# Kernel optimization log

Measured on AMD Instinct MI355X. Metric: run time of the kernel, lower is better.

The kernel has to match this reference:

```python
import jax, jax.numpy as jnp
import numpy as np

N = 100000
E = 1000000
NODE_DIM = 128
EDGE_DIM = 32
HID = 64
HIER = 32
NUM_CLASS = 10
NUM_LAYERS = 3
BN_EPS = 1e-5


def setup_inputs() -> dict:
    key = jax.random.key(0)
    ks = jax.random.split(key, 16)
    s = 0.05
    return {
        "x": jax.random.normal(ks[0], (N, NODE_DIM), jnp.float32),
        "e": jax.random.normal(ks[1], (E, EDGE_DIM), jnp.float32),
        "c": jax.random.normal(ks[2], (N, HIER), jnp.float32),
        "w_node": jax.random.normal(ks[3], (NODE_DIM, HID), jnp.float32) * s,
        "b_node": jnp.zeros((HID,), jnp.float32),
        "w_edge": jax.random.normal(ks[4], (EDGE_DIM, HID), jnp.float32) * s,
        "b_edge": jnp.zeros((HID,), jnp.float32),
        "w_out1": jax.random.normal(ks[5], (HIER + HID, 2 * HID), jnp.float32) * s,
        "b_out1": jnp.zeros((2 * HID,), jnp.float32),
        "bn_gamma": jnp.ones((2 * HID,), jnp.float32),
        "bn_beta": jnp.zeros((2 * HID,), jnp.float32),
        "prelu_a": jnp.asarray(0.25, jnp.float32),
        "w_out2": jax.random.normal(ks[6], (2 * HID, NUM_CLASS), jnp.float32) * s,
        "b_out2": jnp.zeros((NUM_CLASS,), jnp.float32),
        "edge_index": jax.random.randint(ks[7], (2, E), 0, N, jnp.int64),
    }


def reference(x, e, c, w_node, b_node, w_edge, b_edge, w_out1, b_out1,
              bn_gamma, bn_beta, prelu_a, w_out2, b_out2, edge_index):
    n = x.shape[0]
    h = x @ w_node + b_node                      # [N, HID]
    eh = e @ w_edge + b_edge                     # [E, HID]
    src, dst = edge_index[0], edge_index[1]
    loop = jnp.arange(n)
    # add_self_loops + zero self-loop edge_attr (done inside each GCN layer,
    # identical every layer so hoisted)
    src_f = jnp.concatenate([src, loop])
    dst_f = jnp.concatenate([dst, loop])
    e_f = jnp.concatenate([eh, jnp.zeros((n, eh.shape[1]), eh.dtype)], axis=0)
    deg = jax.ops.segment_sum(jnp.ones(dst_f.shape, x.dtype), dst_f, num_segments=n)
    dinv = deg ** -0.5                           # deg >= 1 thanks to self loops
    norm = (dinv[src_f] * dinv[dst_f])[:, None]  # [E+N, 1]
    h_sum = h
    for _ in range(NUM_LAYERS):
        msg = norm * (h[src_f] + e_f)            # gather + edge compute
        h = jax.ops.segment_sum(msg, dst_f, num_segments=n)  # scatter-add
        h = jax.nn.leaky_relu(h, 0.2)
        h_sum = h_sum + h                        # sum over h_list
    z = jnp.concatenate([h_sum, c], axis=-1) @ w_out1 + b_out1
    # BatchNorm1d (training-mode batch statistics, biased variance)
    mu = z.mean(axis=0)
    var = z.var(axis=0)
    z = (z - mu) / jnp.sqrt(var + BN_EPS) * bn_gamma + bn_beta
    z = jnp.where(z > 0, z, prelu_a * z)         # PReLU (single param)
    return z @ w_out2 + b_out2
```

## Files before the change

kernel.cpp:

```cpp
#include <hip/hip_runtime.h>
#include <math.h>

#define N_NODES 100000
#define N_EDGES 1000000
#define HID     64
#define HIER    32
#define NDIM    128
#define EDIM    32
#define K1      96
#define C1      128
#define NCLS    10
#define BN_EPS  1e-5f
#define SCAN_B  98
#define ZTILES  782
#define HTILES2 782

__device__ __forceinline__ unsigned pk_bf16(float a, float b) {
    unsigned ua = __float_as_uint(a);
    ua = (ua + 0x7FFFu + ((ua >> 16) & 1u)) >> 16;
    unsigned ub = __float_as_uint(b);
    ub = (ub + 0x7FFFu + ((ub >> 16) & 1u)) & 0xFFFF0000u;
    return ua | ub;
}
__device__ __forceinline__ float bf_lo(unsigned g) { return __uint_as_float(g << 16); }
__device__ __forceinline__ float bf_hi(unsigned g) { return __uint_as_float(g & 0xFFFF0000u); }


__global__ void k_count(const int* __restrict__ ei, int* __restrict__ cnt) {
    int i = blockIdx.x * blockDim.x + threadIdx.x;
    if (i < N_EDGES) atomicAdd(&cnt[ei[N_EDGES + i]], 1);
}

__global__ void k_scan1(const int* __restrict__ cnt, int* __restrict__ offs,
                        float* __restrict__ dinv, int* __restrict__ bsum) {
    __shared__ int buf[2][1024];
    int t = threadIdx.x, b = blockIdx.x;
    int i = b * 1024 + t;
    int v = (i < N_NODES) ? cnt[i] : 0;
    buf[0][t] = v; __syncthreads();
    int pi = 0;
    for (int off = 1; off < 1024; off <<= 1) {
        int x = buf[pi][t];
        if (t >= off) x += buf[pi][t - off];
        buf[pi ^ 1][t] = x; __syncthreads(); pi ^= 1;
    }
    int incl = buf[pi][t];
    if (i < N_NODES) {
        offs[i] = incl - v;
        dinv[i] = rsqrtf((float)(v + 1));
    }
    if (t == 1023) bsum[b] = incl;
}

__global__ void k_scan2(int* __restrict__ bsum, int nb) {
    __shared__ int buf[2][1024];
    int t = threadIdx.x;
    int v = (t < nb) ? bsum[t] : 0;
    buf[0][t] = v; __syncthreads();
    int pi = 0;
    for (int off = 1; off < 1024; off <<= 1) {
        int x = buf[pi][t];
        if (t >= off) x += buf[pi][t - off];
        buf[pi ^ 1][t] = x; __syncthreads(); pi ^= 1;
    }
    int incl = buf[pi][t];
    if (t < nb) bsum[t] = incl - v;
}

__global__ void k_scan3(const int* __restrict__ bsum, int* __restrict__ offs) {
    int b = blockIdx.x;
    int i = b * 1024 + threadIdx.x;
    if (i < N_NODES) offs[i] += bsum[b];
    if (i == 0) offs[N_NODES] = N_EDGES;
}

__global__ void k_fill(const int* __restrict__ ei, const int* __restrict__ offs,
                       int* __restrict__ cursor, const float* __restrict__ dinv,
                       int4* __restrict__ epk) {
    int i = blockIdx.x * blockDim.x + threadIdx.x;
    if (i >= N_EDGES) return;
    int s = ei[i], d = ei[N_EDGES + i];
    int pos = offs[d] + atomicAdd(&cursor[d], 1);
    epk[pos] = make_int4(s, i, __float_as_int(dinv[s]), 0);
}


__global__ __launch_bounds__(256) void k_conv(const float4* __restrict__ e4,
                                              uint4* __restrict__ eb4) {
    int i = blockIdx.x * 256 + threadIdx.x;
    float4 a = e4[(size_t)2 * i];
    float4 b = e4[(size_t)2 * i + 1];
    uint4 pk;
    pk.x = pk_bf16(a.x, a.y); pk.y = pk_bf16(a.z, a.w);
    pk.z = pk_bf16(b.x, b.y); pk.w = pk_bf16(b.z, b.w);
    eb4[i] = pk;
}

__global__ __launch_bounds__(256) void k_conv2(const float4* __restrict__ c4,
                                               uint2* __restrict__ cb2) {
    int i = blockIdx.x * 256 + threadIdx.x;
    if (i >= N_NODES * 8) return;
    float4 a = c4[i];
    cb2[i] = make_uint2(pk_bf16(a.x, a.y), pk_bf16(a.z, a.w));
}


__global__ __launch_bounds__(256) void k_agg3(const unsigned* __restrict__ ebfu,
                                              const int4* __restrict__ epk,
                                              const int* __restrict__ offs,
                                              const float* __restrict__ dinv,
                                              float* __restrict__ agg,
                                              float* __restrict__ wsumv) {
    int v = (blockIdx.x * 256 + threadIdx.x) >> 4;
    if (v >= N_NODES) return;
    int q = threadIdx.x & 15;
    int start = offs[v], end = offs[v + 1];
    float ax = 0.f, ay = 0.f, wacc = 0.f;
    for (int i = start; i < end; i += 4) {
        int i1 = i + 1, i2 = i + 2, i3 = i + 3;
        int4 p0 = epk[i];
        int4 p1 = (i1 < end) ? epk[i1] : make_int4(0, 0, 0, 0);
        int4 p2 = (i2 < end) ? epk[i2] : make_int4(0, 0, 0, 0);
        int4 p3 = (i3 < end) ? epk[i3] : make_int4(0, 0, 0, 0);
        float n0 = __int_as_float(p0.z), n1 = __int_as_float(p1.z);
        float n2 = __int_as_float(p2.z), n3 = __int_as_float(p3.z);
        unsigned g0 = ebfu[(size_t)p0.y * 16 + q];
        unsigned g1 = ebfu[(size_t)p1.y * 16 + q];
        unsigned g2 = ebfu[(size_t)p2.y * 16 + q];
        unsigned g3 = ebfu[(size_t)p3.y * 16 + q];
        ax += n0 * bf_lo(g0) + n1 * bf_lo(g1) + n2 * bf_lo(g2) + n3 * bf_lo(g3);
        ay += n0 * bf_hi(g0) + n1 * bf_hi(g1) + n2 * bf_hi(g2) + n3 * bf_hi(g3);
        wacc += n0 + n1 + n2 + n3;
    }
    float dv = dinv[v];
    *(float2*)&agg[(size_t)v * EDIM + q * 2] = make_float2(dv * ax, dv * ay);
    if (q == 0) wsumv[v] = dv * wacc;
}


__global__ __launch_bounds__(256) void k_h0t2(const float* __restrict__ x,
                                              const float* __restrict__ w,
                                              const float* __restrict__ bias,
                                              unsigned* __restrict__ hbf) {
    __shared__ __align__(16) unsigned wpk[NDIM * 36];
    __shared__ float xt[128 * 33];
    for (int i = threadIdx.x; i < NDIM * 32; i += 256) {
        int k = i >> 5, j = i & 31;
        wpk[k * 36 + j] = pk_bf16(w[k * HID + 2 * j], w[k * HID + 2 * j + 1]);
    }
    int tid = threadIdx.x;
    int lane = tid & 63, wave = tid >> 6;
    int lr = lane >> 3, lc = lane & 7;
    int rbase = wave * 32 + lr * 4;
    int cbase = lc * 8;
    float bA[8];
    #pragma unroll
    for (int j = 0; j < 8; ++j) bA[j] = bias[cbase + j];
    for (int tile = blockIdx.x; tile < HTILES2; tile += gridDim.x) {
        int row0 = tile * 128;
        float acc[4][8];
        #pragma unroll
        for (int i = 0; i < 4; ++i)
            #pragma unroll
            for (int j = 0; j < 8; ++j) acc[i][j] = 0.f;
        for (int ch = 0; ch < 4; ++ch) {
            __syncthreads();
            #pragma unroll
            for (int p = 0; p < 4; ++p) {
                int idx = p * 256 + tid;
                int row = idx >> 3, kq = idx & 7;
                int gk = ch * 32 + kq * 4;
                float4 v = make_float4(0.f, 0.f, 0.f, 0.f);
                int gr = row0 + row;
                if (gr < N_NODES) v = *(const float4*)&x[(size_t)gr * NDIM + gk];
                float* d = &xt[row * 33 + kq * 4];
                d[0] = v.x; d[1] = v.y; d[2] = v.z; d[3] = v.w;
            }
            __syncthreads();
            for (int k = 0; k < 32; ++k) {
                float u[4];
                #pragma unroll
                for (int i = 0; i < 4; ++i) u[i] = xt[(rbase + i) * 33 + k];
                uint4 wp = *(const uint4*)&wpk[(ch * 32 + k) * 36 + lc * 4];
                float wv[8];
                wv[0] = bf_lo(wp.x); wv[1] = bf_hi(wp.x);
                wv[2] = bf_lo(wp.y); wv[3] = bf_hi(wp.y);
                wv[4] = bf_lo(wp.z); wv[5] = bf_hi(wp.z);
                wv[6] = bf_lo(wp.w); wv[7] = bf_hi(wp.w);
                #pragma unroll
                for (int i = 0; i < 4; ++i)
                    #pragma unroll
                    for (int j = 0; j < 8; ++j) acc[i][j] += u[i] * wv[j];
            }
        }
        #pragma unroll
        for (int i = 0; i < 4; ++i) {
            int gr = row0 + rbase + i;
            if (gr < N_NODES) {
                uint4 pk;
                pk.x = pk_bf16(acc[i][0] + bA[0], acc[i][1] + bA[1]);
                pk.y = pk_bf16(acc[i][2] + bA[2], acc[i][3] + bA[3]);
                pk.z = pk_bf16(acc[i][4] + bA[4], acc[i][5] + bA[5]);
                pk.w = pk_bf16(acc[i][6] + bA[6], acc[i][7] + bA[7]);
                *(uint4*)&hbf[(size_t)gr * 32 + (cbase >> 1)] = pk;
            }
        }
    }
}


__global__ __launch_bounds__(256) void k_se(const float* __restrict__ agg,
                                            const float* __restrict__ wsumv,
                                            const float* __restrict__ we,
                                            const float* __restrict__ be,
                                            unsigned* __restrict__ sebf) {
    int lane = threadIdx.x & 63, wid = threadIdx.x >> 6;
    float wreg[EDIM];
    #pragma unroll
    for (int k = 0; k < EDIM; ++k) wreg[k] = we[k * HID + lane];
    float bl = be[lane];
    for (int v = blockIdx.x * 4 + wid; v < N_NODES; v += gridDim.x * 4) {
        const float4* ar = (const float4*)(agg + (size_t)v * EDIM);
        float acc = wsumv[v] * bl;
        #pragma unroll
        for (int k4 = 0; k4 < EDIM / 4; ++k4) {
            float4 av = ar[k4];
            int k = k4 * 4;
            acc += av.x * wreg[k + 0] + av.y * wreg[k + 1] +
                   av.z * wreg[k + 2] + av.w * wreg[k + 3];
        }
        float partner = __shfl_xor(acc, 1);
        if ((lane & 1) == 0)
            sebf[(size_t)v * 32 + (lane >> 1)] = pk_bf16(acc, partner);
    }
}


__global__ __launch_bounds__(256) void k_layer4(const unsigned* __restrict__ hold,
                                                const unsigned* __restrict__ sebf,
                                                const int4* __restrict__ epk,
                                                const int* __restrict__ offs,
                                                const float* __restrict__ dinv,
                                                unsigned* __restrict__ hnew) {
    int v = (blockIdx.x * 256 + threadIdx.x) >> 4;
    if (v >= N_NODES) return;
    int q = threadIdx.x & 15;
    int start = offs[v], end = offs[v + 1];
    float dv = dinv[v];
    size_t vp = (size_t)v * 16 + q;
    uint2 hv = ((const uint2*)hold)[vp];
    float a0 = dv * bf_lo(hv.x), a1 = dv * bf_hi(hv.x);
    float a2 = dv * bf_lo(hv.y), a3 = dv * bf_hi(hv.y);
    for (int i = start; i < end; i += 8) {
        int idx[8]; float nn[8]; uint2 gg[8];
        #pragma unroll
        for (int u = 0; u < 8; ++u) {
            int ii = i + u;
            int4 p = (ii < end) ? epk[ii] : make_int4(0, 0, 0, 0);
            idx[u] = p.x;
            nn[u]  = __int_as_float(p.z);
        }
        #pragma unroll
        for (int u = 0; u < 8; ++u) gg[u] = ((const uint2*)hold)[(size_t)idx[u] * 16 + q];
        #pragma unroll
        for (int u = 0; u < 8; ++u) {
            a0 += nn[u] * bf_lo(gg[u].x); a1 += nn[u] * bf_hi(gg[u].x);
            a2 += nn[u] * bf_lo(gg[u].y); a3 += nn[u] * bf_hi(gg[u].y);
        }
    }
    uint2 sv = ((const uint2*)sebf)[vp];
    float r0 = bf_lo(sv.x) + dv * a0;
    float r1 = bf_hi(sv.x) + dv * a1;
    float r2 = bf_lo(sv.y) + dv * a2;
    float r3 = bf_hi(sv.y) + dv * a3;
    r0 = (r0 > 0.f) ? r0 : 0.2f * r0;
    r1 = (r1 > 0.f) ? r1 : 0.2f * r1;
    r2 = (r2 > 0.f) ? r2 : 0.2f * r2;
    r3 = (r3 > 0.f) ? r3 : 0.2f * r3;
    ((uint2*)hnew)[vp] = make_uint2(pk_bf16(r0, r1), pk_bf16(r2, r3));
}

__global__ __launch_bounds__(256) void k_layer4s(const unsigned* __restrict__ hold,
                                                 const unsigned* __restrict__ hb0,
                                                 const unsigned* __restrict__ hb1,
                                                 const unsigned* __restrict__ sebf,
                                                 const int4* __restrict__ epk,
                                                 const int* __restrict__ offs,
                                                 const float* __restrict__ dinv,
                                                 unsigned* __restrict__ hnew,
                                                 unsigned* __restrict__ hsbf) {
    int v = (blockIdx.x * 256 + threadIdx.x) >> 4;
    if (v >= N_NODES) return;
    int q = threadIdx.x & 15;
    int start = offs[v], end = offs[v + 1];
    float dv = dinv[v];
    size_t vp = (size_t)v * 16 + q;
    uint2 hv = ((const uint2*)hold)[vp];
    float a0 = dv * bf_lo(hv.x), a1 = dv * bf_hi(hv.x);
    float a2 = dv * bf_lo(hv.y), a3 = dv * bf_hi(hv.y);
    for (int i = start; i < end; i += 8) {
        int idx[8]; float nn[8]; uint2 gg[8];
        #pragma unroll
        for (int u = 0; u < 8; ++u) {
            int ii = i + u;
            int4 p = (ii < end) ? epk[ii] : make_int4(0, 0, 0, 0);
            idx[u] = p.x;
            nn[u]  = __int_as_float(p.z);
        }
        #pragma unroll
        for (int u = 0; u < 8; ++u) gg[u] = ((const uint2*)hold)[(size_t)idx[u] * 16 + q];
        #pragma unroll
        for (int u = 0; u < 8; ++u) {
            a0 += nn[u] * bf_lo(gg[u].x); a1 += nn[u] * bf_hi(gg[u].x);
            a2 += nn[u] * bf_lo(gg[u].y); a3 += nn[u] * bf_hi(gg[u].y);
        }
    }
    uint2 sv = ((const uint2*)sebf)[vp];
    float r0 = bf_lo(sv.x) + dv * a0;
    float r1 = bf_hi(sv.x) + dv * a1;
    float r2 = bf_lo(sv.y) + dv * a2;
    float r3 = bf_hi(sv.y) + dv * a3;
    r0 = (r0 > 0.f) ? r0 : 0.2f * r0;
    r1 = (r1 > 0.f) ? r1 : 0.2f * r1;
    r2 = (r2 > 0.f) ? r2 : 0.2f * r2;
    r3 = (r3 > 0.f) ? r3 : 0.2f * r3;
    ((uint2*)hnew)[vp] = make_uint2(pk_bf16(r0, r1), pk_bf16(r2, r3));
    uint2 g0 = ((const uint2*)hb0)[vp];
    uint2 g1 = ((const uint2*)hb1)[vp];
    float s0 = r0 + bf_lo(g0.x) + bf_lo(g1.x) + bf_lo(hv.x);
    float s1 = r1 + bf_hi(g0.x) + bf_hi(g1.x) + bf_hi(hv.x);
    float s2 = r2 + bf_lo(g0.y) + bf_lo(g1.y) + bf_lo(hv.y);
    float s3 = r3 + bf_hi(g0.y) + bf_hi(g1.y) + bf_hi(hv.y);
    ((uint2*)hsbf)[vp] = make_uint2(pk_bf16(s0, s1), pk_bf16(s2, s3));
}


__global__ __launch_bounds__(256) void k_zstats(const unsigned* __restrict__ hsbf,
                                                const unsigned* __restrict__ cbf,
                                                const float* __restrict__ w1,
                                                const float* __restrict__ b1,
                                                unsigned* __restrict__ zbf,
                                                float* __restrict__ stats) {
    __shared__ __align__(16) unsigned wpk[K1 * 68];
    __shared__ __align__(16) unsigned ut[K1 * 68];
    __shared__ float red[4][64];
    for (int i = threadIdx.x; i < K1 * 64; i += 256) {
        int k = i >> 6, j = i & 63;
        wpk[k * 68 + j] = pk_bf16(w1[k * C1 + 2 * j], w1[k * C1 + 2 * j + 1]);
    }
    int tid = threadIdx.x;
    int lane = tid & 63, wave = tid >> 6;
    int lr = lane >> 3, lc = lane & 7;
    int wr = wave >> 1, wc = wave & 1;
    int rbase = wr * 64 + lr * 8;
    int cbase = wc * 64 + lc * 8;
    int kslot = wave;
    int rp = lane;
    float bA[8];
    #pragma unroll
    for (int j = 0; j < 8; ++j) bA[j] = b1[cbase + j];
    float s[8], q[8];
    #pragma unroll
    for (int j = 0; j < 8; ++j) { s[j] = 0.f; q[j] = 0.f; }

    for (int tile = blockIdx.x; tile < ZTILES; tile += gridDim.x) {
        int row0 = tile * 128;
        __syncthreads();
        {
            int r0g = row0 + 2 * rp, r1g = r0g + 1;
            bool ok0 = r0g < N_NODES, ok1 = r1g < N_NODES;
            #pragma unroll
            for (int kku = 0; kku < 12; ++kku) {
                int ku = kslot * 12 + kku;
                unsigned A = 0u, B = 0u;
                if (ku < 32) {
                    if (ok0) A = hsbf[(size_t)r0g * 32 + ku];
                    if (ok1) B = hsbf[(size_t)r1g * 32 + ku];
                } else {
                    if (ok0) A = cbf[(size_t)r0g * 16 + (ku - 32)];
                    if (ok1) B = cbf[(size_t)r1g * 16 + (ku - 32)];
                }
                int k0 = 2 * ku;
                ut[k0 * 68 + rp]       = (A & 0xFFFFu) | (B << 16);
                ut[(k0 + 1) * 68 + rp] = (A >> 16) | (B & 0xFFFF0000u);
            }
        }
        __syncthreads();
        float acc[8][8];
        #pragma unroll
        for (int i = 0; i < 8; ++i)
            #pragma unroll
            for (int j = 0; j < 8; ++j) acc[i][j] = 0.f;
        for (int k = 0; k < K1; ++k) {
            uint4 up = *(const uint4*)&ut[k * 68 + wr * 32 + lr * 4];
            uint4 wp = *(const uint4*)&wpk[k * 68 + wc * 32 + lc * 4];
            float u[8], wv[8];
            u[0] = bf_lo(up.x); u[1] = bf_hi(up.x);
            u[2] = bf_lo(up.y); u[3] = bf_hi(up.y);
            u[4] = bf_lo(up.z); u[5] = bf_hi(up.z);
            u[6] = bf_lo(up.w); u[7] = bf_hi(up.w);
            wv[0] = bf_lo(wp.x); wv[1] = bf_hi(wp.x);
            wv[2] = bf_lo(wp.y); wv[3] = bf_hi(wp.y);
            wv[4] = bf_lo(wp.z); wv[5] = bf_hi(wp.z);
            wv[6] = bf_lo(wp.w); wv[7] = bf_hi(wp.w);
            #pragma unroll
            for (int i = 0; i < 8; ++i) {
                acc[i][0] += u[i] * wv[0]; acc[i][1] += u[i] * wv[1];
                acc[i][2] += u[i] * wv[2]; acc[i][3] += u[i] * wv[3];
                acc[i][4] += u[i] * wv[4]; acc[i][5] += u[i] * wv[5];
                acc[i][6] += u[i] * wv[6]; acc[i][7] += u[i] * wv[7];
            }
        }
        #pragma unroll
        for (int i = 0; i < 8; ++i) {
            int gr = row0 + rbase + i;
            if (gr < N_NODES) {
                float zz[8];
                #pragma unroll
                for (int j = 0; j < 8; ++j) {
                    zz[j] = acc[i][j] + bA[j];
                    s[j] += zz[j]; q[j] += zz[j] * zz[j];
                }
                uint4 pk;
                pk.x = pk_bf16(zz[0], zz[1]); pk.y = pk_bf16(zz[2], zz[3]);
                pk.z = pk_bf16(zz[4], zz[5]); pk.w = pk_bf16(zz[6], zz[7]);
                *(uint4*)&zbf[(size_t)gr * 64 + (cbase >> 1)] = pk;
            }
        }
    }

    #pragma unroll
    for (int j = 0; j < 8; ++j) {
        s[j] += __shfl_xor(s[j], 8); s[j] += __shfl_xor(s[j], 16); s[j] += __shfl_xor(s[j], 32);
        q[j] += __shfl_xor(q[j], 8); q[j] += __shfl_xor(q[j], 16); q[j] += __shfl_xor(q[j], 32);
    }
    __syncthreads();
    if (lr == 0) {
        #pragma unroll
        for (int j = 0; j < 8; ++j) red[wave][lc * 8 + j] = s[j];
    }
    __syncthreads();
    if (tid < 128) {
        int wc2 = tid >> 6, cl = tid & 63;
        atomicAdd(&stats[wc2 * 64 + cl], red[wc2][cl] + red[wc2 + 2][cl]);
    }
    __syncthreads();
    if (lr == 0) {
        #pragma unroll
        for (int j = 0; j < 8; ++j) red[wave][lc * 8 + j] = q[j];
    }
    __syncthreads();
    if (tid < 128) {
        int wc2 = tid >> 6, cl = tid & 63;
        atomicAdd(&stats[C1 + wc2 * 64 + cl], red[wc2][cl] + red[wc2 + 2][cl]);
    }
}

__global__ void k_ab(const float* __restrict__ stats, const float* __restrict__ gamma,
                     const float* __restrict__ beta, float* __restrict__ ab) {
    int t = threadIdx.x;
    if (t < C1) {
        float mu = stats[t] / (float)N_NODES;
        float var = stats[C1 + t] / (float)N_NODES - mu * mu;
        float inv = rsqrtf(var + BN_EPS);
        float a = gamma[t] * inv;
        ab[t] = a;
        ab[C1 + t] = beta[t] - mu * a;
    }
}


__global__ __launch_bounds__(256) void k_out3(const unsigned* __restrict__ zbf,
                                              const float* __restrict__ ab,
                                              const float* __restrict__ pa,
                                              const float* __restrict__ w2,
                                              const float* __restrict__ b2,
                                              float* __restrict__ out) {
    int v = blockIdx.x * 256 + threadIdx.x;
    if (v >= N_NODES) return;
    float alpha = pa[0];
    float acc[NCLS];
    #pragma unroll
    for (int j = 0; j < NCLS; ++j) acc[j] = b2[j];
    const uint4* zr = (const uint4*)(zbf + (size_t)v * 64);
    #pragma unroll
    for (int pk4 = 0; pk4 < 16; ++pk4) {
        uint4 g = zr[pk4];
        unsigned gw[4] = {g.x, g.y, g.z, g.w};
        #pragma unroll
        for (int w = 0; w < 4; ++w) {
            int d0 = pk4 * 8 + w * 2;
            float p0 = bf_lo(gw[w]) * ab[d0]     + ab[C1 + d0];
            float p1 = bf_hi(gw[w]) * ab[d0 + 1] + ab[C1 + d0 + 1];
            p0 = (p0 > 0.f) ? p0 : alpha * p0;
            p1 = (p1 > 0.f) ? p1 : alpha * p1;
            #pragma unroll
            for (int j = 0; j < NCLS; ++j)
                acc[j] += p0 * w2[d0 * NCLS + j] + p1 * w2[(d0 + 1) * NCLS + j];
        }
    }
    #pragma unroll
    for (int j = 0; j < NCLS; ++j) out[(size_t)v * NCLS + j] = acc[j];
}


extern "C" void kernel_launch(void* const* d_in, const int* in_sizes, int n_in,
                              void* d_out, int out_size, void* d_ws, size_t ws_size,
                              hipStream_t stream) {
    const float* x      = (const float*)d_in[0];
    const float* e      = (const float*)d_in[1];
    const float* c      = (const float*)d_in[2];
    const float* w_node = (const float*)d_in[3];
    const float* b_node = (const float*)d_in[4];
    const float* w_edge = (const float*)d_in[5];
    const float* b_edge = (const float*)d_in[6];
    const float* w_out1 = (const float*)d_in[7];
    const float* b_out1 = (const float*)d_in[8];
    const float* gamma  = (const float*)d_in[9];
    const float* beta   = (const float*)d_in[10];
    const float* pa     = (const float*)d_in[11];
    const float* w_out2 = (const float*)d_in[12];
    const float* b_out2 = (const float*)d_in[13];
    const int*   ei     = (const int*)d_in[14];
    float* out = (float*)d_out;

    char* wsb = (char*)d_ws;
    ushort*   ebf  = (ushort*)wsb;
    unsigned* sebf = (unsigned*)wsb;
    unsigned* zbf  = (unsigned*)(wsb + 12800000);
    size_t off = (64000000 + 255) & ~(size_t)255;
    auto alloc = [&](size_t bytes) {
        void* p = wsb + off;
        off = (off + bytes + 255) & ~(size_t)255;
        return p;
    };
    int*      cnt      = (int*)alloc(4ull * N_NODES);
    int*      offs     = (int*)alloc(4ull * (N_NODES + 1));
    float*    dinv     = (float*)alloc(4ull * N_NODES);
    int*      bsum     = (int*)alloc(4ull * 128);
    int4*     epk      = (int4*)alloc(16ull * N_EDGES);
    float*    agg      = (float*)alloc(4ull * N_NODES * EDIM);
    float*    wsumv    = (float*)alloc(4ull * N_NODES);
    float*    stats    = (float*)alloc(4ull * 256);
    float*    ab       = (float*)alloc(4ull * 256);
    unsigned* hb0      = (unsigned*)alloc(4ull * N_NODES * 32);
    unsigned* hb1      = (unsigned*)alloc(4ull * N_NODES * 32);
    unsigned* hb2      = (unsigned*)alloc(4ull * N_NODES * 32);
    unsigned* hb3      = (unsigned*)alloc(4ull * N_NODES * 32);
    unsigned* cbf      = (unsigned*)alloc(4ull * N_NODES * 16);
    unsigned* hsbf     = (unsigned*)agg;

    hipMemsetAsync(cnt, 0, 4ull * N_NODES, stream);
    hipMemsetAsync(stats, 0, 4ull * 256, stream);

    k_count<<<(N_EDGES + 255) / 256, 256, 0, stream>>>(ei, cnt);
    k_scan1<<<SCAN_B, 1024, 0, stream>>>(cnt, offs, dinv, bsum);
    k_scan2<<<1, 1024, 0, stream>>>(bsum, SCAN_B);
    k_scan3<<<SCAN_B, 1024, 0, stream>>>(bsum, offs);
    hipMemsetAsync(cnt, 0, 4ull * N_NODES, stream);
    k_fill<<<(N_EDGES + 255) / 256, 256, 0, stream>>>(ei, offs, cnt, dinv, epk);

    k_conv<<<15625, 256, 0, stream>>>((const float4*)e, (uint4*)ebf);
    k_agg3<<<N_NODES * 16 / 256, 256, 0, stream>>>((const unsigned*)ebf, epk,
                                                   offs, dinv, agg, wsumv);

    k_se<<<1280, 256, 0, stream>>>(agg, wsumv, w_edge, b_edge, sebf);
    k_conv2<<<(N_NODES * 8 + 255) / 256, 256, 0, stream>>>((const float4*)c, (uint2*)cbf);
    k_h0t2<<<HTILES2, 256, 0, stream>>>(x, w_node, b_node, hb0);

    k_layer4<<<N_NODES * 16 / 256, 256, 0, stream>>>(hb0, sebf, epk, offs, dinv, hb1);
    k_layer4<<<N_NODES * 16 / 256, 256, 0, stream>>>(hb1, sebf, epk, offs, dinv, hb2);
    k_layer4s<<<N_NODES * 16 / 256, 256, 0, stream>>>(hb2, hb0, hb1, sebf, epk, offs,
                                                      dinv, hb3, hsbf);

    k_zstats<<<ZTILES, 256, 0, stream>>>(hsbf, cbf, w_out1, b_out1, zbf, stats);
    k_ab<<<1, 128, 0, stream>>>(stats, gamma, beta, ab);
    k_out3<<<(N_NODES + 255) / 256, 256, 0, stream>>>(zbf, ab, pa, w_out2, b_out2, out);
}
```

Before: 435.0 us.

## Pack CSR edge records into 8 bytes and shrink z-stats row tile

Each CSR edge record is cut from 16 to 8 bytes. The edge id takes 20 bits, the source node id is split across both words, and the normalization factor is stored as bf16. This lowers the memory traffic of the edge-stream reads in the aggregation and all three layer kernels, at the cost of bf16 precision on dinv and some extra bit unpacking. Separately, the z/BN-stats GEMM moves from 128-row to 64-row tiles with smaller shared buffers, doubling the number of blocks to raise occupancy. Each thread now computes fewer accumulators.

```diff
diff --git a/kernel.cpp b/kernel.cpp
--- a/kernel.cpp
+++ b/kernel.cpp
@@ -12,7 +12,7 @@
 #define NCLS    10
 #define BN_EPS  1e-5f
 #define SCAN_B  98
-#define ZTILES  782
+#define ZT64    1563
 #define HTILES2 782
 
 __device__ __forceinline__ unsigned pk_bf16(float a, float b) {
@@ -76,12 +76,14 @@
 
 __global__ void k_fill(const int* __restrict__ ei, const int* __restrict__ offs,
                        int* __restrict__ cursor, const float* __restrict__ dinv,
-                       int4* __restrict__ epk) {
+                       uint2* __restrict__ epk) {
     int i = blockIdx.x * blockDim.x + threadIdx.x;
     if (i >= N_EDGES) return;
     int s = ei[i], d = ei[N_EDGES + i];
     int pos = offs[d] + atomicAdd(&cursor[d], 1);
-    epk[pos] = make_int4(s, i, __float_as_int(dinv[s]), 0);
+    unsigned nhi = pk_bf16(dinv[s], 0.f) << 16;
+    epk[pos] = make_uint2((unsigned)i | ((unsigned)(s & 0xFFF) << 20),
+                          nhi | (unsigned)(s >> 12));
 }
 
 
@@ -106,7 +108,7 @@
 
 
 __global__ __launch_bounds__(256) void k_agg3(const unsigned* __restrict__ ebfu,
-                                              const int4* __restrict__ epk,
+                                              const uint2* __restrict__ epk,
                                               const int* __restrict__ offs,
                                               const float* __restrict__ dinv,
                                               float* __restrict__ agg,
@@ -118,16 +120,16 @@
     float ax = 0.f, ay = 0.f, wacc = 0.f;
     for (int i = start; i < end; i += 4) {
         int i1 = i + 1, i2 = i + 2, i3 = i + 3;
-        int4 p0 = epk[i];
-        int4 p1 = (i1 < end) ? epk[i1] : make_int4(0, 0, 0, 0);
-        int4 p2 = (i2 < end) ? epk[i2] : make_int4(0, 0, 0, 0);
-        int4 p3 = (i3 < end) ? epk[i3] : make_int4(0, 0, 0, 0);
-        float n0 = __int_as_float(p0.z), n1 = __int_as_float(p1.z);
-        float n2 = __int_as_float(p2.z), n3 = __int_as_float(p3.z);
-        unsigned g0 = ebfu[(size_t)p0.y * 16 + q];
-        unsigned g1 = ebfu[(size_t)p1.y * 16 + q];
-        unsigned g2 = ebfu[(size_t)p2.y * 16 + q];
-        unsigned g3 = ebfu[(size_t)p3.y * 16 + q];
+        uint2 p0 = epk[i];
+        uint2 p1 = (i1 < end) ? epk[i1] : make_uint2(0u, 0u);
+        uint2 p2 = (i2 < end) ? epk[i2] : make_uint2(0u, 0u);
+        uint2 p3 = (i3 < end) ? epk[i3] : make_uint2(0u, 0u);
+        float n0 = bf_hi(p0.y), n1 = bf_hi(p1.y);
+        float n2 = bf_hi(p2.y), n3 = bf_hi(p3.y);
+        unsigned g0 = ebfu[(size_t)(p0.x & 0xFFFFFu) * 16 + q];
+        unsigned g1 = ebfu[(size_t)(p1.x & 0xFFFFFu) * 16 + q];
+        unsigned g2 = ebfu[(size_t)(p2.x & 0xFFFFFu) * 16 + q];
+        unsigned g3 = ebfu[(size_t)(p3.x & 0xFFFFFu) * 16 + q];
         ax += n0 * bf_lo(g0) + n1 * bf_lo(g1) + n2 * bf_lo(g2) + n3 * bf_lo(g3);
         ay += n0 * bf_hi(g0) + n1 * bf_hi(g1) + n2 * bf_hi(g2) + n3 * bf_hi(g3);
         wacc += n0 + n1 + n2 + n3;
@@ -236,9 +238,13 @@
 }
 
 
+__device__ __forceinline__ int dec_src(uint2 p) {
+    return (int)(((p.y & 0xFFFFu) << 12) | (p.x >> 20));
+}
+
 __global__ __launch_bounds__(256) void k_layer4(const unsigned* __restrict__ hold,
                                                 const unsigned* __restrict__ sebf,
-                                                const int4* __restrict__ epk,
+                                                const uint2* __restrict__ epk,
                                                 const int* __restrict__ offs,
                                                 const float* __restrict__ dinv,
                                                 unsigned* __restrict__ hnew) {
@@ -256,9 +262,9 @@
         #pragma unroll
         for (int u = 0; u < 8; ++u) {
             int ii = i + u;
-            int4 p = (ii < end) ? epk[ii] : make_int4(0, 0, 0, 0);
-            idx[u] = p.x;
-            nn[u]  = __int_as_float(p.z);
+            uint2 p = (ii < end) ? epk[ii] : make_uint2(0u, 0u);
+            idx[u] = dec_src(p);
+            nn[u]  = bf_hi(p.y);
         }
         #pragma unroll
         for (int u = 0; u < 8; ++u) gg[u] = ((const uint2*)hold)[(size_t)idx[u] * 16 + q];
@@ -284,7 +290,7 @@
                                                  const unsigned* __restrict__ hb0,
                                                  const unsigned* __restrict__ hb1,
                                                  const unsigned* __restrict__ sebf,
-                                                 const int4* __restrict__ epk,
+                                                 const uint2* __restrict__ epk,
                                                  const int* __restrict__ offs,
                                                  const float* __restrict__ dinv,
                                                  unsigned* __restrict__ hnew,
@@ -303,9 +309,9 @@
         #pragma unroll
         for (int u = 0; u < 8; ++u) {
             int ii = i + u;
-            int4 p = (ii < end) ? epk[ii] : make_int4(0, 0, 0, 0);
-            idx[u] = p.x;
-            nn[u]  = __int_as_float(p.z);
+            uint2 p = (ii < end) ? epk[ii] : make_uint2(0u, 0u);
+            idx[u] = dec_src(p);
+            nn[u]  = bf_hi(p.y);
         }
         #pragma unroll
         for (int u = 0; u < 8; ++u) gg[u] = ((const uint2*)hold)[(size_t)idx[u] * 16 + q];
@@ -341,21 +347,20 @@
                                                 const float* __restrict__ b1,
                                                 unsigned* __restrict__ zbf,
                                                 float* __restrict__ stats) {
-    __shared__ __align__(16) unsigned wpk[K1 * 68];
-    __shared__ __align__(16) unsigned ut[K1 * 68];
+    __shared__ __align__(16) unsigned wpk[K1 * 64];
+    __shared__ __align__(16) unsigned ut[K1 * 36];
     __shared__ float red[4][64];
     for (int i = threadIdx.x; i < K1 * 64; i += 256) {
         int k = i >> 6, j = i & 63;
-        wpk[k * 68 + j] = pk_bf16(w1[k * C1 + 2 * j], w1[k * C1 + 2 * j + 1]);
+        wpk[i] = pk_bf16(w1[k * C1 + 2 * j], w1[k * C1 + 2 * j + 1]);
     }
     int tid = threadIdx.x;
     int lane = tid & 63, wave = tid >> 6;
     int lr = lane >> 3, lc = lane & 7;
     int wr = wave >> 1, wc = wave & 1;
-    int rbase = wr * 64 + lr * 8;
+    int rbase = wr * 32 + lr * 4;
     int cbase = wc * 64 + lc * 8;
-    int kslot = wave;
-    int rp = lane;
+    int rp_st = tid & 31, kslot = tid >> 5;
     float bA[8];
     #pragma unroll
     for (int j = 0; j < 8; ++j) bA[j] = b1[cbase + j];
@@ -363,15 +368,15 @@
     #pragma unroll
     for (int j = 0; j < 8; ++j) { s[j] = 0.f; q[j] = 0.f; }
 
-    for (int tile = blockIdx.x; tile < ZTILES; tile += gridDim.x) {
-        int row0 = tile * 128;
+    for (int tile = blockIdx.x; tile < ZT64; tile += gridDim.x) {
+        int row0 = tile * 64;
         __syncthreads();
         {
-            int r0g = row0 + 2 * rp, r1g = r0g + 1;
+            int r0g = row0 + 2 * rp_st, r1g = r0g + 1;
             bool ok0 = r0g < N_NODES, ok1 = r1g < N_NODES;
             #pragma unroll
-            for (int kku = 0; kku < 12; ++kku) {
-                int ku = kslot * 12 + kku;
+            for (int kku = 0; kku < 6; ++kku) {
+                int ku = kslot * 6 + kku;
                 unsigned A = 0u, B = 0u;
                 if (ku < 32) {
                     if (ok0) A = hsbf[(size_t)r0g * 32 + ku];
@@ -381,30 +386,28 @@
                     if (ok1) B = cbf[(size_t)r1g * 16 + (ku - 32)];
                 }
                 int k0 = 2 * ku;
-                ut[k0 * 68 + rp]       = (A & 0xFFFFu) | (B << 16);
-                ut[(k0 + 1) * 68 + rp] = (A >> 16) | (B & 0xFFFF0000u);
+                ut[k0 * 36 + rp_st]       = (A & 0xFFFFu) | (B << 16);
+                ut[(k0 + 1) * 36 + rp_st] = (A >> 16) | (B & 0xFFFF0000u);
             }
         }
         __syncthreads();
-        float acc[8][8];
-        #pragma unroll
-        for (int i = 0; i < 8; ++i)
+        float acc[4][8];
+        #pragma unroll
+        for (int i = 0; i < 4; ++i)
             #pragma unroll
             for (int j = 0; j < 8; ++j) acc[i][j] = 0.f;
         for (int k = 0; k < K1; ++k) {
-            uint4 up = *(const uint4*)&ut[k * 68 + wr * 32 + lr * 4];
-            uint4 wp = *(const uint4*)&wpk[k * 68 + wc * 32 + lc * 4];
-            float u[8], wv[8];
+            uint2 up = *(const uint2*)&ut[k * 36 + wr * 16 + lr * 2];
+            uint4 wp = *(const uint4*)&wpk[k * 64 + wc * 32 + lc * 4];
+            float u[4], wv[8];
             u[0] = bf_lo(up.x); u[1] = bf_hi(up.x);
             u[2] = bf_lo(up.y); u[3] = bf_hi(up.y);
-            u[4] = bf_lo(up.z); u[5] = bf_hi(up.z);
-            u[6] = bf_lo(up.w); u[7] = bf_hi(up.w);
             wv[0] = bf_lo(wp.x); wv[1] = bf_hi(wp.x);
             wv[2] = bf_lo(wp.y); wv[3] = bf_hi(wp.y);
             wv[4] = bf_lo(wp.z); wv[5] = bf_hi(wp.z);
             wv[6] = bf_lo(wp.w); wv[7] = bf_hi(wp.w);
             #pragma unroll
-            for (int i = 0; i < 8; ++i) {
+            for (int i = 0; i < 4; ++i) {
                 acc[i][0] += u[i] * wv[0]; acc[i][1] += u[i] * wv[1];
                 acc[i][2] += u[i] * wv[2]; acc[i][3] += u[i] * wv[3];
                 acc[i][4] += u[i] * wv[4]; acc[i][5] += u[i] * wv[5];
@@ -412,7 +415,7 @@
             }
         }
         #pragma unroll
-        for (int i = 0; i < 8; ++i) {
+        for (int i = 0; i < 4; ++i) {
             int gr = row0 + rbase + i;
             if (gr < N_NODES) {
                 float zz[8];
@@ -538,7 +541,7 @@
     int*      offs     = (int*)alloc(4ull * (N_NODES + 1));
     float*    dinv     = (float*)alloc(4ull * N_NODES);
     int*      bsum     = (int*)alloc(4ull * 128);
-    int4*     epk      = (int4*)alloc(16ull * N_EDGES);
+    uint2*    epk      = (uint2*)alloc(8ull * N_EDGES);
     float*    agg      = (float*)alloc(4ull * N_NODES * EDIM);
     float*    wsumv    = (float*)alloc(4ull * N_NODES);
     float*    stats    = (float*)alloc(4ull * 256);
@@ -573,7 +576,7 @@
     k_layer4s<<<N_NODES * 16 / 256, 256, 0, stream>>>(hb2, hb0, hb1, sebf, epk, offs,
                                                       dinv, hb3, hsbf);
 
-    k_zstats<<<ZTILES, 256, 0, stream>>>(hsbf, cbf, w_out1, b_out1, zbf, stats);
+    k_zstats<<<ZT64, 256, 0, stream>>>(hsbf, cbf, w_out1, b_out1, zbf, stats);
     k_ab<<<1, 128, 0, stream>>>(stats, gamma, beta, ab);
     k_out3<<<(N_NODES + 255) / 256, 256, 0, stream>>>(zbf, ab, pa, w_out2, b_out2, out);
 }
```

Result: slower. 443.8 us (+2.0%).
